# Performance work log

Measured on AMD Instinct MI355X. Metric: run time of the kernel, lower is better.

Reference implementation:

```python
import jax, jax.numpy as jnp
import numpy as np

# module init constants
HEAVY_RATIO = 0.1
RECENT_RATIO = 0.1


def setup_inputs() -> dict:
    key = jax.random.key(0)
    attn_weights = jax.random.normal(key, (2, 32, 1024, 1024), dtype=jnp.float32)
    return {"attn_weights": attn_weights, "group_size": 8}


def reference(attn_weights, group_size):
    # First-forward path of CachedHeavyRecentAttentionMasker (cached_indices is None).
    bs, head, q_len, k_len = attn_weights.shape
    dtype = attn_weights.dtype
    min_value = jnp.finfo(dtype).min
    num_groups = head // group_size

    # [bs, ng, gs, q, k]
    attn_g = attn_weights.reshape(bs, num_groups, group_size, q_len, k_len)
    tmp_attn = jax.nn.softmax(attn_g.astype(jnp.float32), axis=-1).astype(dtype)
    importance = tmp_attn.sum(axis=-2)  # [bs, ng, gs, k]

    heavy_budget = max(1, min(int(HEAVY_RATIO * k_len), k_len))
    _, topk_idx = jax.lax.top_k(importance, heavy_budget)  # [bs, ng, gs, hb]
    # scatter True at topk indices -> boolean heavy mask per head
    heavy_mask_head = jnp.any(jax.nn.one_hot(topk_idx, k_len, dtype=jnp.bool_), axis=-2)  # [bs, ng, gs, k]
    heavy_mask_group = jnp.any(heavy_mask_head, axis=2)  # [bs, ng, k]

    # first call: final mask is just the heavy-hitter group mask
    final_mask_group = heavy_mask_group

    i = jnp.arange(q_len)[:, None]
    j = jnp.arange(k_len)[None, :]
    causal = j <= i  # [q, k]
    recent_budget = int(RECENT_RATIO * k_len)
    if recent_budget > 0:
        recent_band = causal & (j >= i - recent_budget)
    else:
        recent_band = i == j

    # broadcast group mask to per-head [bs, head, q, k]
    keep = jnp.broadcast_to(
        final_mask_group[:, :, None, None, :],
        (bs, num_groups, group_size, q_len, k_len),
    ).reshape(bs, head, q_len, k_len)
    keep = (keep & causal) | recent_band

    fetch_mask = jnp.where(keep, jnp.zeros((), dtype), jnp.full((), min_value, dtype))
    density = keep.sum().astype(jnp.float32) / (bs * head) / (q_len * (q_len + 1) / 2)
    return fetch_mask, density
```

## Files before the change

### kernel.cpp

```cpp
#include <hip/hip_runtime.h>
#include <float.h>
#include <stdint.h>

#define QLEN 1024
#define KLEN 1024
#define NHEADS 64
#define NGROUPS 8
#define CH 16
#define HEAVY_BUDGET 102
#define RECENT 102
#define RECENT_SUM 100219LL

#define MASK_VAL __uint_as_float(0xFF7F0000u)

typedef float v4f __attribute__((ext_vector_type(4)));
typedef unsigned long long v2u __attribute__((ext_vector_type(2)));

#define PARTIAL_F  0
#define HEADMASK_F (NHEADS * CH * KLEN)
#define HEAVY_F    (HEADMASK_F + (NHEADS * KLEN) / 4)
#define GCOUNT_F   (HEAVY_F + (NGROUPS * KLEN) / 4)
#define TAIL_LO    1040
#define TAIL_HI    1042

__global__ __launch_bounds__(256) void k_importance(const float* __restrict__ attn,
                                                    float* __restrict__ partial) {
  const int blk   = blockIdx.x;
  const int head  = blk >> 4;
  const int chunk = blk & (CH - 1);
  const int tid   = threadIdx.x;
  const int wave  = tid >> 6;
  const int lane  = tid & 63;

  float acc[16];
#pragma unroll
  for (int t = 0; t < 16; ++t) acc[t] = 0.f;

  const v4f* head4 = (const v4f*)(attn + (size_t)head * QLEN * KLEN);
  const int q0 = chunk * (QLEN / CH) + wave * 16;

  v4f a[4], b[4];
  {
    const v4f* rowA = head4 + (size_t)q0 * (KLEN / 4);
    const v4f* rowB = rowA + (KLEN / 4);
#pragma unroll
    for (int c = 0; c < 4; ++c) { a[c] = rowA[c * 64 + lane]; b[c] = rowB[c * 64 + lane]; }
  }

  for (int rp = 0; rp < 8; ++rp) {
    v4f na[4], nb[4];
    if (rp < 7) {
      const v4f* nA = head4 + (size_t)(q0 + 2 * rp + 2) * (KLEN / 4);
      const v4f* nB = nA + (KLEN / 4);
#pragma unroll
      for (int c = 0; c < 4; ++c) { na[c] = nA[c * 64 + lane]; nb[c] = nB[c * 64 + lane]; }
    }

    float za = 0.f, zb = 0.f;
#pragma unroll
    for (int c = 0; c < 4; ++c)
#pragma unroll
      for (int d = 0; d < 4; ++d) {
        a[c][d] = __expf(a[c][d]);
        b[c][d] = __expf(b[c][d]);
        za += a[c][d];
        zb += b[c][d];
      }

#pragma unroll
    for (int s = 32; s >= 1; s >>= 1) {
      za += __shfl_xor(za, s, 64);
      zb += __shfl_xor(zb, s, 64);
    }

    const float iza = 1.0f / za, izb = 1.0f / zb;
#pragma unroll
    for (int c = 0; c < 4; ++c)
#pragma unroll
      for (int d = 0; d < 4; ++d)
        acc[c * 4 + d] += a[c][d] * iza + b[c][d] * izb;

#pragma unroll
    for (int c = 0; c < 4; ++c) { a[c] = na[c]; b[c] = nb[c]; }
  }

  __shared__ float lds[4][KLEN];
#pragma unroll
  for (int c = 0; c < 4; ++c)
#pragma unroll
    for (int d = 0; d < 4; ++d)
      lds[wave][(c * 64 + lane) * 4 + d] = acc[c * 4 + d];
  __syncthreads();

  v4f* outp = (v4f*)(partial + ((size_t)head * CH + chunk) * KLEN);
  const int k0 = tid * 4;
  v4f o;
#pragma unroll
  for (int d = 0; d < 4; ++d)
    o[d] = (lds[0][k0 + d] + lds[1][k0 + d]) + (lds[2][k0 + d] + lds[3][k0 + d]);
  outp[tid] = o;
}

__global__ __launch_bounds__(256) void k_rank(const float* __restrict__ partial,
                                              unsigned char* __restrict__ head_mask) {
  const int head = blockIdx.x >> 2;
  const int seg  = blockIdx.x & 3;
  const int t    = threadIdx.x;

  __shared__ unsigned long long keys[KLEN];

  const float* base = partial + (size_t)head * CH * KLEN;
#pragma unroll
  for (int j = 0; j < 4; ++j) {
    const int k = j * 256 + t;
    float s = 0.f;
#pragma unroll
    for (int c = 0; c < CH; ++c) s += base[c * KLEN + k];
    keys[k] = ((unsigned long long)__float_as_uint(s) << 10) |
              (unsigned long long)(KLEN - 1 - k);
  }
  __syncthreads();

  const int kk = seg * 256 + t;
  const unsigned long long mykey = keys[kk];
  const v2u* k2 = (const v2u*)keys;
  int rank = 0;
#pragma unroll 8
  for (int u = 0; u < KLEN / 2; ++u) {
    const v2u w = k2[u];
    rank += (w[0] > mykey) ? 1 : 0;
    rank += (w[1] > mykey) ? 1 : 0;
  }

  head_mask[head * KLEN + kk] = (rank < HEAVY_BUDGET) ? 1 : 0;
}

__global__ __launch_bounds__(1024) void k_combine(const unsigned char* __restrict__ head_mask,
                                                  unsigned char* __restrict__ heavy,
                                                  long long* __restrict__ gcount) {
  const int grp = blockIdx.x;
  const int k   = threadIdx.x;

  unsigned char m = 0;
#pragma unroll
  for (int hh = 0; hh < 8; ++hh) m |= head_mask[(grp * 8 + hh) * KLEN + k];
  heavy[grp * KLEN + k] = m;

  const int umax = QLEN - 1 - (RECENT + 1);
  int contrib = (m && k <= umax) ? (umax + 1 - k) : 0;

  __shared__ int red[16];
  int sum = contrib;
#pragma unroll
  for (int s = 32; s >= 1; s >>= 1) sum += __shfl_xor(sum, s, 64);
  if ((k & 63) == 0) red[k >> 6] = sum;
  __syncthreads();
  if (k < 16) {
    int x = red[k];
#pragma unroll
    for (int s = 8; s >= 1; s >>= 1) x += __shfl_xor(x, s, 64);
    if (k == 0) gcount[grp] = 8LL * (RECENT_SUM + (long long)x);
  }
}

__global__ __launch_bounds__(256) void k_mask_main(const unsigned char* __restrict__ heavy,
                                                   float* __restrict__ out) {
  const int tid  = threadIdx.x;
  const int row0 = blockIdx.x * 8;
  const int grp  = row0 >> 13;
  const float mv = MASK_VAL;
  const uchar4 hv = ((const uchar4*)(heavy + grp * KLEN))[tid];
  const int hx = hv.x, hy = hv.y, hz = hv.z, hw = hv.w;
  const int j0 = tid * 4;

#pragma unroll
  for (int r = 0; r < 8; ++r) {
    const int row = row0 + r;
    if (row >= TAIL_LO && row <= TAIL_HI) continue;
    const int i  = row & (QLEN - 1);
    const int lo = i - RECENT;
    v4f o;
    o[0] = ((j0 + 0) <= i && (hx || (j0 + 0) >= lo)) ? 0.f : mv;
    o[1] = ((j0 + 1) <= i && (hy || (j0 + 1) >= lo)) ? 0.f : mv;
    o[2] = ((j0 + 2) <= i && (hz || (j0 + 2) >= lo)) ? 0.f : mv;
    o[3] = ((j0 + 3) <= i && (hw || (j0 + 3) >= lo)) ? 0.f : mv;
    __builtin_nontemporal_store(o, (v4f*)(out + (size_t)row * KLEN) + tid);
  }
}

__global__ __launch_bounds__(256) void k_tail(const long long* __restrict__ gcount,
                                              float* __restrict__ out) {
  const int tid = threadIdx.x;
  const float mv = MASK_VAL;

  float dens = 0.f;
  if (tid == 0) {
    long long s = 0;
    for (int g = 0; g < NGROUPS; ++g) s += gcount[g];
    float f = (float)s;
    f = f / 64.0f;
    f = f / 524800.0f;
    dens = f;
  }
  __syncthreads();

  const int j0 = tid * 4;
  for (int row = TAIL_LO; row <= TAIL_HI; ++row) {
    const int i = row & (QLEN - 1);
    v4f o;
    o[0] = ((j0 + 0) <= i) ? 0.f : mv;
    o[1] = ((j0 + 1) <= i) ? 0.f : mv;
    o[2] = ((j0 + 2) <= i) ? 0.f : mv;
    o[3] = ((j0 + 3) <= i) ? 0.f : mv;
    ((v4f*)(out + (size_t)row * KLEN))[tid] = o;
  }
  if (tid == 0) out[(size_t)NHEADS * QLEN * KLEN] = dens;
}

extern "C" void kernel_launch(void* const* d_in, const int* in_sizes, int n_in,
                              void* d_out, int out_size, void* d_ws, size_t ws_size,
                              hipStream_t stream) {
  const float* attn = (const float*)d_in[0];
  float* out = (float*)d_out;

  float*         partial   = out + PARTIAL_F;
  unsigned char* head_mask = (unsigned char*)(out + HEADMASK_F);
  unsigned char* heavy     = (unsigned char*)(out + HEAVY_F);
  long long*     gcount    = (long long*)(out + GCOUNT_F);

  k_importance<<<NHEADS * CH, 256, 0, stream>>>(attn, partial);
  k_rank<<<NHEADS * 4, 256, 0, stream>>>(partial, head_mask);
  k_combine<<<NGROUPS, 1024, 0, stream>>>(head_mask, heavy, gcount);
  k_mask_main<<<8192, 256, 0, stream>>>(heavy, out);
  k_tail<<<1, 256, 0, stream>>>(gcount, out);
}
```

Baseline: 115.9 us.

## Fuse rank, group-combine and density into one kernel using workspace scratch

Moves intermediate buffers from the output tensor into the provided workspace. This removes the separate tail kernel and the skipped-row handling. Rank, combine and the density reduction are merged into one kernel that uses atomic counters as a grid-wide barrier, cutting five launches to three. The spin-wait assumes all 256 blocks are co-resident. It also adds atomic polling latency, and it only runs when the workspace is large enough.

After: 131.1 us. +13.1%, slower.

```diff
diff --git a/kernel.cpp b/kernel.cpp
--- a/kernel.cpp
+++ b/kernel.cpp
@@ -14,7 +14,10 @@
 #define MASK_VAL __uint_as_float(0xFF7F0000u)
 
 typedef float v4f __attribute__((ext_vector_type(4)));
+typedef unsigned long long u64;
 typedef unsigned long long v2u __attribute__((ext_vector_type(2)));
+
+#define WS_NEED (73728u + (size_t)NHEADS * CH * KLEN * 4u)
 
 #define PARTIAL_F  0
 #define HEADMASK_F (NHEADS * CH * KLEN)
@@ -24,7 +27,10 @@
 #define TAIL_HI    1042
 
 __global__ __launch_bounds__(256) void k_importance(const float* __restrict__ attn,
-                                                    float* __restrict__ partial) {
+                                                    float* __restrict__ partial,
+                                                    int* __restrict__ counters) {
+  if (counters && blockIdx.x == 0 && threadIdx.x < 2) counters[threadIdx.x] = 0;
+
   const int blk   = blockIdx.x;
   const int head  = blk >> 4;
   const int chunk = blk & (CH - 1);
@@ -101,70 +107,103 @@
   outp[tid] = o;
 }
 
-__global__ __launch_bounds__(256) void k_rank(const float* __restrict__ partial,
-                                              unsigned char* __restrict__ head_mask) {
-  const int head = blockIdx.x >> 2;
-  const int seg  = blockIdx.x & 3;
+__global__ __launch_bounds__(256) void k_select(const float* __restrict__ partial,
+                                                unsigned char* __restrict__ head_mask,
+                                                unsigned char* __restrict__ heavy,
+                                                long long* __restrict__ gcount,
+                                                int* __restrict__ counters,
+                                                float* __restrict__ out) {
+  const int blk  = blockIdx.x;
+  const int head = blk >> 2;
+  const int seg  = blk & 3;
   const int t    = threadIdx.x;
 
-  __shared__ unsigned long long keys[KLEN];
-
-  const float* base = partial + (size_t)head * CH * KLEN;
-#pragma unroll
-  for (int j = 0; j < 4; ++j) {
-    const int k = j * 256 + t;
-    float s = 0.f;
-#pragma unroll
-    for (int c = 0; c < CH; ++c) s += base[c * KLEN + k];
-    keys[k] = ((unsigned long long)__float_as_uint(s) << 10) |
-              (unsigned long long)(KLEN - 1 - k);
-  }
-  __syncthreads();
-
-  const int kk = seg * 256 + t;
-  const unsigned long long mykey = keys[kk];
-  const v2u* k2 = (const v2u*)keys;
-  int rank = 0;
+  __shared__ u64 keys[KLEN];
+  __shared__ int red[4];
+
+  {
+    const v4f* base4 = (const v4f*)(partial + (size_t)head * CH * KLEN);
+    v4f s4 = {0.f, 0.f, 0.f, 0.f};
+#pragma unroll
+    for (int c = 0; c < CH; ++c) {
+      const v4f v = base4[c * (KLEN / 4) + t];
+#pragma unroll
+      for (int d = 0; d < 4; ++d) s4[d] += v[d];
+    }
+#pragma unroll
+    for (int d = 0; d < 4; ++d) {
+      const int k = 4 * t + d;
+      keys[k] = ((u64)__float_as_uint(s4[d]) << 10) | (u64)(KLEN - 1 - k);
+    }
+  }
+  __syncthreads();
+
+  {
+    const int kk = seg * 256 + t;
+    const u64 mykey = keys[kk];
+    const v2u* k2 = (const v2u*)keys;
+    int rank = 0;
 #pragma unroll 8
-  for (int u = 0; u < KLEN / 2; ++u) {
-    const v2u w = k2[u];
-    rank += (w[0] > mykey) ? 1 : 0;
-    rank += (w[1] > mykey) ? 1 : 0;
-  }
-
-  head_mask[head * KLEN + kk] = (rank < HEAVY_BUDGET) ? 1 : 0;
-}
-
-__global__ __launch_bounds__(1024) void k_combine(const unsigned char* __restrict__ head_mask,
-                                                  unsigned char* __restrict__ heavy,
-                                                  long long* __restrict__ gcount) {
-  const int grp = blockIdx.x;
-  const int k   = threadIdx.x;
-
-  unsigned char m = 0;
-#pragma unroll
-  for (int hh = 0; hh < 8; ++hh) m |= head_mask[(grp * 8 + hh) * KLEN + k];
-  heavy[grp * KLEN + k] = m;
-
-  const int umax = QLEN - 1 - (RECENT + 1);
-  int contrib = (m && k <= umax) ? (umax + 1 - k) : 0;
-
-  __shared__ int red[16];
-  int sum = contrib;
-#pragma unroll
-  for (int s = 32; s >= 1; s >>= 1) sum += __shfl_xor(sum, s, 64);
-  if ((k & 63) == 0) red[k >> 6] = sum;
-  __syncthreads();
-  if (k < 16) {
-    int x = red[k];
-#pragma unroll
-    for (int s = 8; s >= 1; s >>= 1) x += __shfl_xor(x, s, 64);
-    if (k == 0) gcount[grp] = 8LL * (RECENT_SUM + (long long)x);
+    for (int u = 0; u < KLEN / 2; ++u) {
+      const v2u w = k2[u];
+      rank += (w[0] > mykey) ? 1 : 0;
+      rank += (w[1] > mykey) ? 1 : 0;
+    }
+    head_mask[head * KLEN + kk] = (rank < HEAVY_BUDGET) ? 1 : 0;
+  }
+
+  __threadfence();
+  __syncthreads();
+  if (t == 0) atomicAdd(&counters[0], 1);
+  if (blk >= NGROUPS) return;
+
+  if (t == 0) { while (atomicAdd(&counters[0], 0) < 256) __builtin_amdgcn_s_sleep(2); }
+  __syncthreads();
+  __threadfence();
+
+  {
+    const int grp = blk;
+    const unsigned int* hm32 = (const unsigned int*)head_mask;
+    unsigned int m = 0;
+#pragma unroll
+    for (int hh = 0; hh < 8; ++hh) m |= hm32[((grp * 8 + hh) * KLEN) >> 2 | t];
+    ((unsigned int*)heavy)[((grp * KLEN) >> 2) + t] = m;
+
+    const int umax = QLEN - 1 - (RECENT + 1);
+    int contrib = 0;
+#pragma unroll
+    for (int d = 0; d < 4; ++d) {
+      const int k = 4 * t + d;
+      const int mb = (m >> (8 * d)) & 1;
+      if (mb && k <= umax) contrib += umax + 1 - k;
+    }
+#pragma unroll
+    for (int s = 32; s >= 1; s >>= 1) contrib += __shfl_xor(contrib, s, 64);
+    if ((t & 63) == 0) red[t >> 6] = contrib;
+    __syncthreads();
+    if (t == 0) {
+      gcount[grp] = 8LL * (RECENT_SUM + (long long)(red[0] + red[1] + red[2] + red[3]));
+      __threadfence();
+      atomicAdd(&counters[1], 1);
+    }
+  }
+  if (blk != 0) return;
+
+  if (t == 0) {
+    while (atomicAdd(&counters[1], 0) < NGROUPS) __builtin_amdgcn_s_sleep(2);
+    __threadfence();
+    long long s = 0;
+    for (int g = 0; g < NGROUPS; ++g) s += gcount[g];
+    float f = (float)s;
+    f = f / 64.0f;
+    f = f / 524800.0f;
+    out[(size_t)NHEADS * QLEN * KLEN] = f;
   }
 }
 
 __global__ __launch_bounds__(256) void k_mask_main(const unsigned char* __restrict__ heavy,
-                                                   float* __restrict__ out) {
+                                                   float* __restrict__ out,
+                                                   int skip_tail) {
   const int tid  = threadIdx.x;
   const int row0 = blockIdx.x * 8;
   const int grp  = row0 >> 13;
@@ -176,7 +215,7 @@
 #pragma unroll
   for (int r = 0; r < 8; ++r) {
     const int row = row0 + r;
-    if (row >= TAIL_LO && row <= TAIL_HI) continue;
+    if (skip_tail && row >= TAIL_LO && row <= TAIL_HI) continue;
     const int i  = row & (QLEN - 1);
     const int lo = i - RECENT;
     v4f o;
@@ -185,6 +224,66 @@
     o[2] = ((j0 + 2) <= i && (hz || (j0 + 2) >= lo)) ? 0.f : mv;
     o[3] = ((j0 + 3) <= i && (hw || (j0 + 3) >= lo)) ? 0.f : mv;
     __builtin_nontemporal_store(o, (v4f*)(out + (size_t)row * KLEN) + tid);
+  }
+}
+
+__global__ __launch_bounds__(256) void k_rank(const float* __restrict__ partial,
+                                              unsigned char* __restrict__ head_mask) {
+  const int head = blockIdx.x >> 2;
+  const int seg  = blockIdx.x & 3;
+  const int t    = threadIdx.x;
+
+  __shared__ u64 keys[KLEN];
+
+  const float* base = partial + (size_t)head * CH * KLEN;
+#pragma unroll
+  for (int j = 0; j < 4; ++j) {
+    const int k = j * 256 + t;
+    float s = 0.f;
+#pragma unroll
+    for (int c = 0; c < CH; ++c) s += base[c * KLEN + k];
+    keys[k] = ((u64)__float_as_uint(s) << 10) | (u64)(KLEN - 1 - k);
+  }
+  __syncthreads();
+
+  const int kk = seg * 256 + t;
+  const u64 mykey = keys[kk];
+  const v2u* k2 = (const v2u*)keys;
+  int rank = 0;
+#pragma unroll 8
+  for (int u = 0; u < KLEN / 2; ++u) {
+    const v2u w = k2[u];
+    rank += (w[0] > mykey) ? 1 : 0;
+    rank += (w[1] > mykey) ? 1 : 0;
+  }
+  head_mask[head * KLEN + kk] = (rank < HEAVY_BUDGET) ? 1 : 0;
+}
+
+__global__ __launch_bounds__(1024) void k_combine(const unsigned char* __restrict__ head_mask,
+                                                  unsigned char* __restrict__ heavy,
+                                                  long long* __restrict__ gcount) {
+  const int grp = blockIdx.x;
+  const int k   = threadIdx.x;
+
+  unsigned char m = 0;
+#pragma unroll
+  for (int hh = 0; hh < 8; ++hh) m |= head_mask[(grp * 8 + hh) * KLEN + k];
+  heavy[grp * KLEN + k] = m;
+
+  const int umax = QLEN - 1 - (RECENT + 1);
+  int contrib = (m && k <= umax) ? (umax + 1 - k) : 0;
+
+  __shared__ int red[16];
+  int sum = contrib;
+#pragma unroll
+  for (int s = 32; s >= 1; s >>= 1) sum += __shfl_xor(sum, s, 64);
+  if ((k & 63) == 0) red[k >> 6] = sum;
+  __syncthreads();
+  if (k < 16) {
+    int x = red[k];
+#pragma unroll
+    for (int s = 8; s >= 1; s >>= 1) x += __shfl_xor(x, s, 64);
+    if (k == 0) gcount[grp] = 8LL * (RECENT_SUM + (long long)x);
   }
 }
 
@@ -222,15 +321,28 @@
                               hipStream_t stream) {
   const float* attn = (const float*)d_in[0];
   float* out = (float*)d_out;
-
-  float*         partial   = out + PARTIAL_F;
-  unsigned char* head_mask = (unsigned char*)(out + HEADMASK_F);
-  unsigned char* heavy     = (unsigned char*)(out + HEAVY_F);
-  long long*     gcount    = (long long*)(out + GCOUNT_F);
-
-  k_importance<<<NHEADS * CH, 256, 0, stream>>>(attn, partial);
-  k_rank<<<NHEADS * 4, 256, 0, stream>>>(partial, head_mask);
-  k_combine<<<NGROUPS, 1024, 0, stream>>>(head_mask, heavy, gcount);
-  k_mask_main<<<8192, 256, 0, stream>>>(heavy, out);
-  k_tail<<<1, 256, 0, stream>>>(gcount, out);
-}
+  char*  ws  = (char*)d_ws;
+
+  if (ws && ws_size >= WS_NEED) {
+    int*           counters  = (int*)ws;
+    long long*     gcount    = (long long*)(ws + 64);
+    unsigned char* heavy     = (unsigned char*)(ws + 128);
+    unsigned char* head_mask = (unsigned char*)(ws + 8320);
+    float*         partial   = (float*)(ws + 73728);
+
+    k_importance<<<NHEADS * CH, 256, 0, stream>>>(attn, partial, counters);
+    k_select<<<256, 256, 0, stream>>>(partial, head_mask, heavy, gcount, counters, out);
+    k_mask_main<<<8192, 256, 0, stream>>>(heavy, out, 0);
+  } else {
+    float*         partial   = out + PARTIAL_F;
+    unsigned char* head_mask = (unsigned char*)(out + HEADMASK_F);
+    unsigned char* heavy     = (unsigned char*)(out + HEAVY_F);
+    long long*     gcount    = (long long*)(out + GCOUNT_F);
+
+    k_importance<<<NHEADS * CH, 256, 0, stream>>>(attn, partial, nullptr);
+    k_rank<<<NHEADS * 4, 256, 0, stream>>>(partial, head_mask);
+    k_combine<<<NGROUPS, 1024, 0, stream>>>(head_mask, heavy, gcount);
+    k_mask_main<<<8192, 256, 0, stream>>>(heavy, out, 1);
+    k_tail<<<1, 256, 0, stream>>>(gcount, out);
+  }
+}
```

## Fuse mask writes for heavy-independent columns into importance pass, use workspace scratch

Applied to the files above, without the earlier changes.

When a workspace is available, scratch buffers move out of the output into the workspace. The importance kernel then writes the part of each output row that does not depend on the heavy set (columns from i-RECENT onward) while streaming the input. A smaller fix kernel later writes only the left columns that depend on the heavy mask, and it also writes the density. This overlaps part of the 256MB output write with the input read and drops the tail kernel, but the importance kernel gains extra store traffic and becomes more complex.

New measurement: 128.0 us. +10.4%, slower.

```diff
diff --git a/kernel.cpp b/kernel.cpp
--- a/kernel.cpp
+++ b/kernel.cpp
@@ -14,7 +14,11 @@
 #define MASK_VAL __uint_as_float(0xFF7F0000u)
 
 typedef float v4f __attribute__((ext_vector_type(4)));
+typedef unsigned long long u64;
 typedef unsigned long long v2u __attribute__((ext_vector_type(2)));
+
+
+#define WS_NEED (73728u + (size_t)NHEADS * CH * KLEN * 4u)
 
 #define PARTIAL_F  0
 #define HEADMASK_F (NHEADS * CH * KLEN)
@@ -23,8 +27,10 @@
 #define TAIL_LO    1040
 #define TAIL_HI    1042
 
+template <bool WM>
 __global__ __launch_bounds__(256) void k_importance(const float* __restrict__ attn,
-                                                    float* __restrict__ partial) {
+                                                    float* __restrict__ partial,
+                                                    float* __restrict__ out) {
   const int blk   = blockIdx.x;
   const int head  = blk >> 4;
   const int chunk = blk & (CH - 1);
@@ -80,6 +86,30 @@
       for (int d = 0; d < 4; ++d)
         acc[c * 4 + d] += a[c][d] * iza + b[c][d] * izb;
 
+    if constexpr (WM) {
+      const float mv = MASK_VAL;
+#pragma unroll
+      for (int rr = 0; rr < 2; ++rr) {
+        const int i    = q0 + 2 * rp + rr;
+        const int lo   = i - RECENT;
+        const int nvec = (lo > 0) ? ((lo + 3) >> 2) : 0;
+        v4f* rowOut = (v4f*)(out + ((size_t)head * QLEN + i) * KLEN);
+#pragma unroll
+        for (int c = 0; c < 4; ++c) {
+          const int vidx = c * 64 + lane;
+          if (vidx >= nvec) {
+            const int k0 = vidx * 4;
+            v4f o;
+            o[0] = (k0 + 0 <= i) ? 0.f : mv;
+            o[1] = (k0 + 1 <= i) ? 0.f : mv;
+            o[2] = (k0 + 2 <= i) ? 0.f : mv;
+            o[3] = (k0 + 3 <= i) ? 0.f : mv;
+            __builtin_nontemporal_store(o, rowOut + vidx);
+          }
+        }
+      }
+    }
+
 #pragma unroll
     for (int c = 0; c < 4; ++c) { a[c] = na[c]; b[c] = nb[c]; }
   }
@@ -107,7 +137,7 @@
   const int seg  = blockIdx.x & 3;
   const int t    = threadIdx.x;
 
-  __shared__ unsigned long long keys[KLEN];
+  __shared__ u64 keys[KLEN];
 
   const float* base = partial + (size_t)head * CH * KLEN;
 #pragma unroll
@@ -116,13 +146,12 @@
     float s = 0.f;
 #pragma unroll
     for (int c = 0; c < CH; ++c) s += base[c * KLEN + k];
-    keys[k] = ((unsigned long long)__float_as_uint(s) << 10) |
-              (unsigned long long)(KLEN - 1 - k);
+    keys[k] = ((u64)__float_as_uint(s) << 10) | (u64)(KLEN - 1 - k);
   }
   __syncthreads();
 
   const int kk = seg * 256 + t;
-  const unsigned long long mykey = keys[kk];
+  const u64 mykey = keys[kk];
   const v2u* k2 = (const v2u*)keys;
   int rank = 0;
 #pragma unroll 8
@@ -131,7 +160,6 @@
     rank += (w[0] > mykey) ? 1 : 0;
     rank += (w[1] > mykey) ? 1 : 0;
   }
-
   head_mask[head * KLEN + kk] = (rank < HEAVY_BUDGET) ? 1 : 0;
 }
 
@@ -163,7 +191,44 @@
   }
 }
 
-__global__ __launch_bounds__(256) void k_mask_main(const unsigned char* __restrict__ heavy,
+__global__ __launch_bounds__(256) void k_fix(const unsigned char* __restrict__ heavy,
+                                             const long long* __restrict__ gcount,
+                                             float* __restrict__ out) {
+  const int tid  = threadIdx.x;
+  const int row0 = blockIdx.x * 8;
+  const int grp  = row0 >> 13;
+  const float mv = MASK_VAL;
+
+  if (blockIdx.x == 0 && tid == 0) {
+    long long s = 0;
+    for (int g = 0; g < NGROUPS; ++g) s += gcount[g];
+    float f = (float)s;
+    f = f / 64.0f;
+    f = f / 524800.0f;
+    out[(size_t)NHEADS * QLEN * KLEN] = f;
+  }
+
+  const uchar4 hv = ((const uchar4*)(heavy + grp * KLEN))[tid];
+  const int j0 = tid * 4;
+
+#pragma unroll
+  for (int r = 0; r < 8; ++r) {
+    const int row = row0 + r;
+    const int i   = row & (QLEN - 1);
+    const int lo  = i - RECENT;
+    const int nvec = (lo > 0) ? ((lo + 3) >> 2) : 0;
+    if (tid < nvec) {
+      v4f o;
+      o[0] = ((j0 + 0) <= i && (hv.x || (j0 + 0) >= lo)) ? 0.f : mv;
+      o[1] = ((j0 + 1) <= i && (hv.y || (j0 + 1) >= lo)) ? 0.f : mv;
+      o[2] = ((j0 + 2) <= i && (hv.z || (j0 + 2) >= lo)) ? 0.f : mv;
+      o[3] = ((j0 + 3) <= i && (hv.w || (j0 + 3) >= lo)) ? 0.f : mv;
+      __builtin_nontemporal_store(o, (v4f*)(out + (size_t)row * KLEN) + tid);
+    }
+  }
+}
+
+__global__ __launch_bounds__(256) void k_mask_full(const unsigned char* __restrict__ heavy,
                                                    float* __restrict__ out) {
   const int tid  = threadIdx.x;
   const int row0 = blockIdx.x * 8;
@@ -222,15 +287,28 @@
                               hipStream_t stream) {
   const float* attn = (const float*)d_in[0];
   float* out = (float*)d_out;
-
-  float*         partial   = out + PARTIAL_F;
-  unsigned char* head_mask = (unsigned char*)(out + HEADMASK_F);
-  unsigned char* heavy     = (unsigned char*)(out + HEAVY_F);
-  long long*     gcount    = (long long*)(out + GCOUNT_F);
-
-  k_importance<<<NHEADS * CH, 256, 0, stream>>>(attn, partial);
-  k_rank<<<NHEADS * 4, 256, 0, stream>>>(partial, head_mask);
-  k_combine<<<NGROUPS, 1024, 0, stream>>>(head_mask, heavy, gcount);
-  k_mask_main<<<8192, 256, 0, stream>>>(heavy, out);
-  k_tail<<<1, 256, 0, stream>>>(gcount, out);
-}
+  char*  ws  = (char*)d_ws;
+
+  if (ws && ws_size >= WS_NEED) {
+    long long*     gcount    = (long long*)(ws + 64);
+    unsigned char* heavy     = (unsigned char*)(ws + 128);
+    unsigned char* head_mask = (unsigned char*)(ws + 8320);
+    float*         partial   = (float*)(ws + 73728);
+
+    k_importance<true><<<NHEADS * CH, 256, 0, stream>>>(attn, partial, out);
+    k_rank<<<NHEADS * 4, 256, 0, stream>>>(partial, head_mask);
+    k_combine<<<NGROUPS, 1024, 0, stream>>>(head_mask, heavy, gcount);
+    k_fix<<<8192, 256, 0, stream>>>(heavy, gcount, out);
+  } else {
+    float*         partial   = out + PARTIAL_F;
+    unsigned char* head_mask = (unsigned char*)(out + HEADMASK_F);
+    unsigned char* heavy     = (unsigned char*)(out + HEAVY_F);
+    long long*     gcount    = (long long*)(out + GCOUNT_F);
+
+    k_importance<false><<<NHEADS * CH, 256, 0, stream>>>(attn, partial, nullptr);
+    k_rank<<<NHEADS * 4, 256, 0, stream>>>(partial, head_mask);
+    k_combine<<<NGROUPS, 1024, 0, stream>>>(head_mask, heavy, gcount);
+    k_mask_full<<<8192, 256, 0, stream>>>(heavy, out);
+    k_tail<<<1, 256, 0, stream>>>(gcount, out);
+  }
+}
```
